# Kernel optimization log

Hardware: AMD Instinct MI355X
Metric: run time of the kernel (lower is better)

## Reference

```python
import jax, jax.numpy as jnp
import numpy as np

NBINS = 256  # skimage threshold_otsu default
RGB_W = jnp.array([0.2989, 0.5870, 0.1140], dtype=jnp.float32)  # tf.image.rgb_to_grayscale weights


def threshold_otsu(img):
    """Global Otsu threshold over all pixels, matching skimage.filters.threshold_otsu."""
    vmin = img.min()
    vmax = img.max()
    edges = jnp.linspace(vmin, vmax, NBINS + 1)
    centers = (edges[:-1] + edges[1:]) * 0.5
    hist = jnp.histogram(img.ravel(), bins=edges)[0].astype(jnp.float32)
    # class probabilities / cumulative weights
    w1 = jnp.cumsum(hist)                      # weight of class <= t
    w2 = jnp.cumsum(hist[::-1])[::-1]          # weight of class > t
    hc = hist * centers
    s1 = jnp.cumsum(hc)
    s2 = jnp.cumsum(hc[::-1])[::-1]
    m1 = s1 / jnp.maximum(w1, 1.0)
    m2 = s2 / jnp.maximum(w2, 1.0)
    # inter-class variance at each split point
    var12 = w1[:-1] * w2[1:] * (m1[:-1] - m2[1:]) ** 2
    idx = jnp.argmax(var12)
    return centers[idx]


def setup_inputs() -> dict:
    key = jax.random.key(0)
    inputs = jax.random.uniform(key, (32, 128, 2048, 3), dtype=jnp.float32)
    return {"inputs": inputs}


def reference(inputs) -> jnp.ndarray:
    # rgb_to_grayscale on first 3 channels, keep channel dim -> [B,H,W,1]
    gray = jnp.einsum('bhwc,c->bhw', inputs[..., :3].astype(jnp.float32), RGB_W)[..., None]
    thresh = threshold_otsu(gray)
    binarized = (gray > thresh).astype(jnp.float32)   # [B,H,W,1]
    # channels == 3 -> tile grayscale binarization back to 3 channels
    binarized = jnp.tile(binarized, (1, 1, 1, 3))
    return binarized
```

## Files before the change

### kernel.cpp

```cpp
#include <hip/hip_runtime.h>

static constexpr int HIST_OFF    = 2;
static constexpr int EDGES_OFF   = 258;
static constexpr int VMIN_OFF    = 515;
static constexpr int DELTA_OFF   = 516;
static constexpr int INVD_OFF    = 517;
static constexpr int THRESH_OFF  = 518;
static constexpr int SCRATCH_OFF = 1024;
static constexpr size_t GRAY_BYTE_OFF = 32768;

typedef float nfloat4 __attribute__((ext_vector_type(4)));

__device__ __forceinline__ unsigned fkey(float x) {
    unsigned u = __float_as_uint(x);
    return (u & 0x80000000u) ? ~u : (u | 0x80000000u);
}
__device__ __forceinline__ float keyf(unsigned k) {
    return (k & 0x80000000u) ? __uint_as_float(k & 0x7FFFFFFFu)
                             : __uint_as_float(~k);
}
__device__ __forceinline__ float gray1(float r, float g, float b) {
    float t0 = __fmul_rn(r, 0.2989f);
    float t1 = __fmul_rn(g, 0.5870f);
    float t2 = __fmul_rn(b, 0.1140f);
    return __fadd_rn(__fadd_rn(t0, t1), t2);
}

__device__ __forceinline__ void bin4(float x0, float x1, float x2, float x3,
                                     const float* eds, float vmin, float invd,
                                     unsigned* lh) {
    float xs[4] = {x0, x1, x2, x3};
#pragma unroll
    for (int j = 0; j < 4; ++j) {
        float x = xs[j];
        int b = (int)(__fmul_rn(__fsub_rn(x, vmin), invd));
        b = b < 0 ? 0 : (b > 255 ? 255 : b);
        while (b < 255 && x >= eds[b + 1]) ++b;
        while (b > 0 && x < eds[b]) --b;
        atomicAdd(&lh[b], 1u);
    }
}

__device__ __forceinline__ void reduce_pairs(const unsigned* __restrict__ wsu,
                                             int npairs, int t,
                                             unsigned& mn, unsigned& mx,
                                             unsigned* rmn, unsigned* rmx) {
    mn = 0xFFFFFFFFu; mx = 0u;
    for (int i = t; i < npairs; i += 256) {
        mn = min(mn, wsu[SCRATCH_OFF + 2 * i]);
        mx = max(mx, wsu[SCRATCH_OFF + 2 * i + 1]);
    }
    for (int off = 32; off > 0; off >>= 1) {
        mn = min(mn, (unsigned)__shfl_xor((int)mn, off, 64));
        mx = max(mx, (unsigned)__shfl_xor((int)mx, off, 64));
    }
    const int w = t >> 6;
    if ((t & 63) == 0) { rmn[w] = mn; rmx[w] = mx; }
    __syncthreads();
    mn = min(min(rmn[0], rmn[1]), min(rmn[2], rmn[3]));
    mx = max(max(rmx[0], rmx[1]), max(rmx[2], rmx[3]));
}


__global__ void __launch_bounds__(256)
gray_minmax_lds(const float* __restrict__ in, float* __restrict__ gray,
                unsigned* __restrict__ wsu, int npix4) {
    __shared__ float4 sb[4][2][192];
    __shared__ unsigned smn[4], smx[4];
    const float4* __restrict__ in4 = (const float4*)in;
    float4* __restrict__ gray4 = (float4*)gray;
    const int lane = threadIdx.x & 63;
    const int w = threadIdx.x >> 6;
    const int gw = blockIdx.x * 4 + w;
    const size_t base = (size_t)gw * 768;
    unsigned mn = 0xFFFFFFFFu, mx = 0u;

    if (blockIdx.x == 0) wsu[HIST_OFF + threadIdx.x] = 0u;

    float4 a0 = in4[base + lane];
    float4 a1 = in4[base + 64 + lane];
    float4 a2 = in4[base + 128 + lane];
    __builtin_amdgcn_sched_barrier(0);
    sb[w][0][lane]       = a0;
    sb[w][0][64 + lane]  = a1;
    sb[w][0][128 + lane] = a2;
    a0 = in4[base + 192 + lane];
    a1 = in4[base + 256 + lane];
    a2 = in4[base + 320 + lane];
    __builtin_amdgcn_sched_barrier(0);

#pragma unroll
    for (int t = 0; t < 4; ++t) {
        const int cb = t & 1;
        float4 c0 = sb[w][cb][3 * lane + 0];
        float4 c1 = sb[w][cb][3 * lane + 1];
        float4 c2 = sb[w][cb][3 * lane + 2];
        float g0 = gray1(c0.x, c0.y, c0.z);
        float g1 = gray1(c0.w, c1.x, c1.y);
        float g2 = gray1(c1.z, c1.w, c2.x);
        float g3 = gray1(c2.y, c2.z, c2.w);
        gray4[(size_t)gw * 256 + t * 64 + lane] = make_float4(g0, g1, g2, g3);
        unsigned k0 = fkey(g0), k1 = fkey(g1), k2 = fkey(g2), k3 = fkey(g3);
        mn = min(mn, min(min(k0, k1), min(k2, k3)));
        mx = max(mx, max(max(k0, k1), max(k2, k3)));
        if (t < 3) {
            sb[w][cb ^ 1][lane]       = a0;
            sb[w][cb ^ 1][64 + lane]  = a1;
            sb[w][cb ^ 1][128 + lane] = a2;
            if (t < 2) {
                a0 = in4[base + (size_t)(t + 2) * 192 + lane];
                a1 = in4[base + (size_t)(t + 2) * 192 + 64 + lane];
                a2 = in4[base + (size_t)(t + 2) * 192 + 128 + lane];
            }
            __builtin_amdgcn_sched_barrier(0);
        }
    }
    for (int off = 32; off > 0; off >>= 1) {
        mn = min(mn, (unsigned)__shfl_xor((int)mn, off, 64));
        mx = max(mx, (unsigned)__shfl_xor((int)mx, off, 64));
    }
    if (lane == 0) { smn[w] = mn; smx[w] = mx; }
    __syncthreads();
    if (threadIdx.x == 0) {
        mn = min(min(smn[0], smn[1]), min(smn[2], smn[3]));
        mx = max(max(smx[0], smx[1]), max(smx[2], smx[3]));
        wsu[SCRATCH_OFF + 2 * blockIdx.x]     = mn;
        wsu[SCRATCH_OFF + 2 * blockIdx.x + 1] = mx;
    }
}

__global__ void __launch_bounds__(256)
hist_fused(const float* __restrict__ gray, unsigned* __restrict__ wsu,
           int npairs, int npix4) {
    __shared__ float eds[257];
    __shared__ unsigned lh[256];
    __shared__ unsigned rmn[4], rmx[4];
    const int t = threadIdx.x;
    unsigned mn, mx;
    reduce_pairs(wsu, npairs, t, mn, mx, rmn, rmx);
    const float vmin = keyf(mn);
    const float vmax = keyf(mx);
    const float delta = __fdiv_rn(__fsub_rn(vmax, vmin), 256.0f);
    const float invd = (delta > 0.0f) ? __fdiv_rn(1.0f, delta) : 0.0f;
    eds[t] = __fadd_rn(vmin, __fmul_rn((float)t, delta));
    if (t == 0) eds[256] = vmax;
    lh[t] = 0u;
    __syncthreads();

    const int stride = gridDim.x * 256;
    const int base = blockIdx.x * 256 + t;
    float4 g[8];
#pragma unroll
    for (int j = 0; j < 8; ++j) g[j] = ((const float4*)gray)[base + j * stride];
#pragma unroll
    for (int j = 0; j < 8; ++j)
        bin4(g[j].x, g[j].y, g[j].z, g[j].w, eds, vmin, invd, lh);
    __syncthreads();
    if (lh[t] != 0u) atomicAdd(&wsu[HIST_OFF + t], lh[t]);
}

__global__ void __launch_bounds__(256)
binarize_fused(const float* __restrict__ gray, const unsigned* __restrict__ wsu,
               float* __restrict__ out, int npairs, int npix4) {
    __shared__ float eds[257];
    __shared__ float histf[256], centers[256];
    __shared__ float w1a[256], s1a[256], w2a[256], s2a[256];
    __shared__ unsigned rmn[4], rmx[4];
    __shared__ float rbv[4];
    __shared__ int rbi[4];
    __shared__ float sthresh;
    const int t = threadIdx.x;
    const int lane = t & 63;
    const int w = t >> 6;

    unsigned mn, mx;
    reduce_pairs(wsu, npairs, t, mn, mx, rmn, rmx);
    const float vmin = keyf(mn);
    const float vmax = keyf(mx);
    const float delta = __fdiv_rn(__fsub_rn(vmax, vmin), 256.0f);
    eds[t] = __fadd_rn(vmin, __fmul_rn((float)t, delta));
    if (t == 0) eds[256] = vmax;
    histf[t] = (float)wsu[HIST_OFF + t];
    __syncthreads();
    centers[t] = __fmul_rn(__fadd_rn(eds[t], eds[t + 1]), 0.5f);
    __syncthreads();
    if (t == 0) {
        float ww = 0.0f, ss = 0.0f;
        for (int k = 255; k >= 0; --k) {
            ww = __fadd_rn(ww, histf[k]);
            ss = __fadd_rn(ss, __fmul_rn(histf[k], centers[k]));
            w2a[k] = ww;
            s2a[k] = ss;
        }
        ww = 0.0f; ss = 0.0f;
        for (int k = 0; k < 255; ++k) {
            ww = __fadd_rn(ww, histf[k]);
            ss = __fadd_rn(ss, __fmul_rn(histf[k], centers[k]));
            w1a[k] = ww;
            s1a[k] = ss;
        }
    }
    __syncthreads();
    float v = -1.0f;
    int ti = 256;
    if (t < 255) {
        float m1 = __fdiv_rn(s1a[t], fmaxf(w1a[t], 1.0f));
        float m2 = __fdiv_rn(s2a[t + 1], fmaxf(w2a[t + 1], 1.0f));
        float d  = __fsub_rn(m1, m2);
        v  = __fmul_rn(__fmul_rn(w1a[t], w2a[t + 1]), __fmul_rn(d, d));
        ti = t;
    }
    for (int off = 32; off > 0; off >>= 1) {
        float ov = __shfl_xor(v, off, 64);
        int oi = __shfl_xor(ti, off, 64);
        if (ov > v || (ov == v && oi < ti)) { v = ov; ti = oi; }
    }
    if (lane == 0) { rbv[w] = v; rbi[w] = ti; }
    __syncthreads();
    if (t == 0) {
        float bv = rbv[0]; int bi = rbi[0];
        for (int k = 1; k < 4; ++k)
            if (rbv[k] > bv || (rbv[k] == bv && rbi[k] < bi)) {
                bv = rbv[k]; bi = rbi[k];
            }
        sthresh = centers[bi];
    }
    __syncthreads();
    const float thr = sthresh;

    const nfloat4* gray4 = (const nfloat4*)gray;
    nfloat4* out4 = (nfloat4*)out;
    const int gw = blockIdx.x * 4 + w;
    const int ma = lane / 3,         qa = lane % 3;
    const int mb = (64 + lane) / 3,  qb = (64 + lane) % 3;
    const int mc = (128 + lane) / 3, qc = (128 + lane) % 3;
#pragma unroll
    for (int r = 0; r < 8; ++r) {
        const int gbase = gw * 512 + r * 64;
        nfloat4 gg = gray4[gbase + lane];
        unsigned u = (gg.x > thr ? 1u : 0u) |
                     (gg.y > thr ? 0x100u : 0u) |
                     (gg.z > thr ? 0x10000u : 0u) |
                     (gg.w > thr ? 0x1000000u : 0u);
        const size_t rb = 3 * (size_t)gbase;
#pragma unroll
        for (int k = 0; k < 3; ++k) {
            int m = (k == 0) ? ma : (k == 1) ? mb : mc;
            int q = (k == 0) ? qa : (k == 1) ? qb : qc;
            unsigned x = (unsigned)__builtin_amdgcn_ds_bpermute(4 * m, (int)u);
            float h0 = (x & 0xffu)       ? 1.0f : 0.0f;
            float h1 = (x & 0xff00u)     ? 1.0f : 0.0f;
            float h2 = (x & 0xff0000u)   ? 1.0f : 0.0f;
            float h3 = (x & 0xff000000u) ? 1.0f : 0.0f;
            nfloat4 o;
            o.x = (q == 0) ? h0 : (q == 1) ? h1 : h2;
            o.y = (q == 0) ? h0 : (q == 1) ? h1 : h3;
            o.z = (q == 0) ? h0 : (q == 1) ? h2 : h3;
            o.w = (q == 0) ? h1 : (q == 1) ? h2 : h3;
            __builtin_nontemporal_store(o, &out4[rb + 64 * k + lane]);
        }
    }
}


__global__ void init_kernel(unsigned* __restrict__ wsu) {
    int i = threadIdx.x;
    if (i < 256) wsu[HIST_OFF + i] = 0u;
    if (i == 0) { wsu[0] = 0xFFFFFFFFu; wsu[1] = 0u; }
}

__global__ void __launch_bounds__(256)
gray_minmax_generic(const float* __restrict__ in, float* __restrict__ gray,
                    unsigned* __restrict__ wsu, int npix4) {
    __shared__ unsigned smn[4], smx[4];
    const float4* in4 = (const float4*)in;
    const int stride = gridDim.x * blockDim.x;
    unsigned mn = 0xFFFFFFFFu, mx = 0u;
    for (int t = blockIdx.x * blockDim.x + threadIdx.x; t < npix4; t += stride) {
        const float4* p = in4 + (size_t)t * 3;
        float4 c0 = p[0], c1 = p[1], c2 = p[2];
        float g0 = gray1(c0.x, c0.y, c0.z);
        float g1 = gray1(c0.w, c1.x, c1.y);
        float g2 = gray1(c1.z, c1.w, c2.x);
        float g3 = gray1(c2.y, c2.z, c2.w);
        if (gray) ((float4*)gray)[t] = make_float4(g0, g1, g2, g3);
        unsigned k0 = fkey(g0), k1 = fkey(g1), k2 = fkey(g2), k3 = fkey(g3);
        mn = min(mn, min(min(k0, k1), min(k2, k3)));
        mx = max(mx, max(max(k0, k1), max(k2, k3)));
    }
    for (int off = 32; off > 0; off >>= 1) {
        mn = min(mn, (unsigned)__shfl_xor((int)mn, off, 64));
        mx = max(mx, (unsigned)__shfl_xor((int)mx, off, 64));
    }
    int wave = threadIdx.x >> 6;
    if ((threadIdx.x & 63) == 0) { smn[wave] = mn; smx[wave] = mx; }
    __syncthreads();
    if (threadIdx.x == 0) {
        mn = min(min(smn[0], smn[1]), min(smn[2], smn[3]));
        mx = max(max(smx[0], smx[1]), max(smx[2], smx[3]));
        atomicMin(&wsu[0], mn);
        atomicMax(&wsu[1], mx);
    }
}

__global__ void edges_kernel(unsigned* __restrict__ wsu,
                             float* __restrict__ wsf, int nblk) {
    __shared__ unsigned rmn[4], rmx[4];
    const int i = threadIdx.x;
    unsigned mn = 0xFFFFFFFFu, mx = 0u;
    if (nblk > 0) {
        for (int b = i; b < nblk; b += 256) {
            mn = min(mn, wsu[SCRATCH_OFF + 2 * b]);
            mx = max(mx, wsu[SCRATCH_OFF + 2 * b + 1]);
        }
        for (int off = 32; off > 0; off >>= 1) {
            mn = min(mn, (unsigned)__shfl_xor((int)mn, off, 64));
            mx = max(mx, (unsigned)__shfl_xor((int)mx, off, 64));
        }
        const int w = i >> 6;
        if ((i & 63) == 0) { rmn[w] = mn; rmx[w] = mx; }
        __syncthreads();
        mn = min(min(rmn[0], rmn[1]), min(rmn[2], rmn[3]));
        mx = max(max(rmx[0], rmx[1]), max(rmx[2], rmx[3]));
    } else {
        mn = wsu[0];
        mx = wsu[1];
    }
    const float vmin = keyf(mn);
    const float vmax = keyf(mx);
    const float delta = __fdiv_rn(__fsub_rn(vmax, vmin), 256.0f);
    wsf[EDGES_OFF + i] = __fadd_rn(vmin, __fmul_rn((float)i, delta));
    if (i == 0) {
        wsf[EDGES_OFF + 256] = vmax;
        wsf[VMIN_OFF]  = vmin;
        wsf[DELTA_OFF] = delta;
        wsf[INVD_OFF]  = (delta > 0.0f) ? __fdiv_rn(1.0f, delta) : 0.0f;
    }
}

__global__ void __launch_bounds__(256)
hist_kernel(const float* __restrict__ gray, const float* __restrict__ in,
            const float* __restrict__ wsf, unsigned* __restrict__ wsu,
            int npix4) {
    __shared__ float eds[257];
    __shared__ unsigned lh[256];
    for (int i = threadIdx.x; i < 257; i += blockDim.x)
        eds[i] = wsf[EDGES_OFF + i];
    if (threadIdx.x < 256) lh[threadIdx.x] = 0u;
    __syncthreads();
    const float vmin = eds[0];
    const float invd = wsf[INVD_OFF];
    const int stride = gridDim.x * blockDim.x;
    const int base = blockIdx.x * blockDim.x + threadIdx.x;
    for (int t = base; t < npix4; t += stride) {
        float4 g4;
        if (gray) g4 = ((const float4*)gray)[t];
        else {
            const float4* p = (const float4*)in + (size_t)t * 3;
            float4 c0 = p[0], c1 = p[1], c2 = p[2];
            g4 = make_float4(gray1(c0.x, c0.y, c0.z), gray1(c0.w, c1.x, c1.y),
                             gray1(c1.z, c1.w, c2.x), gray1(c2.y, c2.z, c2.w));
        }
        bin4(g4.x, g4.y, g4.z, g4.w, eds, vmin, invd, lh);
    }
    __syncthreads();
    if (threadIdx.x < 256 && lh[threadIdx.x] != 0u)
        atomicAdd(&wsu[HIST_OFF + threadIdx.x], lh[threadIdx.x]);
}

__global__ void otsu_kernel(const unsigned* __restrict__ wsu,
                            float* __restrict__ wsf) {
    __shared__ float histf[256];
    __shared__ float centers[256];
    __shared__ float w2a[256];
    __shared__ float s2a[256];
    int i = threadIdx.x;
    float e0 = wsf[EDGES_OFF + i];
    float e1 = wsf[EDGES_OFF + i + 1];
    centers[i] = __fmul_rn(__fadd_rn(e0, e1), 0.5f);
    histf[i] = (float)wsu[HIST_OFF + i];
    __syncthreads();
    if (i == 0) {
        float w = 0.0f, s = 0.0f;
        for (int t = 255; t >= 0; --t) {
            w = __fadd_rn(w, histf[t]);
            s = __fadd_rn(s, __fmul_rn(histf[t], centers[t]));
            w2a[t] = w;
            s2a[t] = s;
        }
        float w1 = 0.0f, s1 = 0.0f, best = -1.0f;
        int bidx = 0;
        for (int t = 0; t < 255; ++t) {
            w1 = __fadd_rn(w1, histf[t]);
            s1 = __fadd_rn(s1, __fmul_rn(histf[t], centers[t]));
            float m1 = __fdiv_rn(s1, fmaxf(w1, 1.0f));
            float m2 = __fdiv_rn(s2a[t + 1], fmaxf(w2a[t + 1], 1.0f));
            float d  = __fsub_rn(m1, m2);
            float v  = __fmul_rn(__fmul_rn(w1, w2a[t + 1]), __fmul_rn(d, d));
            if (v > best) { best = v; bidx = t; }
        }
        wsf[THRESH_OFF] = centers[bidx];
    }
}

__global__ void __launch_bounds__(256)
binarize_generic(const float* __restrict__ gray, const float* __restrict__ in,
                 const float* __restrict__ wsf, float* __restrict__ out,
                 int npix4) {
    const float thr = wsf[THRESH_OFF];
    const int stride = gridDim.x * blockDim.x;
    nfloat4* out4 = (nfloat4*)out;
    for (int t = blockIdx.x * blockDim.x + threadIdx.x; t < npix4; t += stride) {
        float4 g4;
        if (gray) g4 = ((const float4*)gray)[t];
        else {
            const float4* p = (const float4*)in + (size_t)t * 3;
            float4 c0 = p[0], c1 = p[1], c2 = p[2];
            g4 = make_float4(gray1(c0.x, c0.y, c0.z), gray1(c0.w, c1.x, c1.y),
                             gray1(c1.z, c1.w, c2.x), gray1(c2.y, c2.z, c2.w));
        }
        float b0 = (g4.x > thr) ? 1.0f : 0.0f;
        float b1 = (g4.y > thr) ? 1.0f : 0.0f;
        float b2 = (g4.z > thr) ? 1.0f : 0.0f;
        float b3 = (g4.w > thr) ? 1.0f : 0.0f;
        nfloat4* o = out4 + (size_t)t * 3;
        o[0] = (nfloat4){b0, b0, b0, b1};
        o[1] = (nfloat4){b1, b1, b2, b2};
        o[2] = (nfloat4){b2, b3, b3, b3};
    }
}

static void launch_fallback(const float* in, float* out, unsigned* wsu,
                            float* wsf, float* gray, int npix4,
                            hipStream_t stream) {
    hipLaunchKernelGGL(init_kernel, dim3(1), dim3(256), 0, stream, wsu);
    hipLaunchKernelGGL(gray_minmax_generic, dim3(2048), dim3(256), 0,
                       stream, in, gray, wsu, npix4);
    hipLaunchKernelGGL(edges_kernel, dim3(1), dim3(256), 0, stream, wsu, wsf,
                       0);
    hipLaunchKernelGGL(hist_kernel, dim3(1024), dim3(256), 0, stream,
                       gray, in, wsf, wsu, npix4);
    hipLaunchKernelGGL(otsu_kernel, dim3(1), dim3(256), 0, stream, wsu, wsf);
    hipLaunchKernelGGL(binarize_generic, dim3(2048), dim3(256), 0, stream,
                       gray, in, wsf, out, npix4);
}

extern "C" void kernel_launch(void* const* d_in, const int* in_sizes, int n_in,
                              void* d_out, int out_size, void* d_ws,
                              size_t ws_size, hipStream_t stream) {
    const float* in = (const float*)d_in[0];
    float* out = (float*)d_out;
    int npix  = out_size / 3;
    int npix4 = npix / 4;
    unsigned* wsu = (unsigned*)d_ws;
    float* wsf = (float*)d_ws;
    size_t need = GRAY_BYTE_OFF + (size_t)npix * sizeof(float);
    float* gray = (ws_size >= need)
                      ? (float*)((char*)d_ws + GRAY_BYTE_OFF)
                      : nullptr;

    const bool fast = gray && (npix4 % 2048 == 0);
    if (fast) {
        const int npairs = npix4 / 1024;
        const int nb2 = npix4 / 2048;
        hipLaunchKernelGGL(gray_minmax_lds, dim3(npairs), dim3(256), 0,
                           stream, in, gray, wsu, npix4);
        hipLaunchKernelGGL(hist_fused, dim3(nb2), dim3(256), 0, stream,
                           gray, wsu, npairs, npix4);
        hipLaunchKernelGGL(binarize_fused, dim3(nb2), dim3(256), 0, stream,
                           gray, wsu, out, npairs, npix4);
    } else {
        launch_fallback(in, out, wsu, wsf, gray, npix4, stream);
    }
}
```

Measured before the change: 237.8 us.

## Fuse grayscale, histogram, Otsu and binarize into one persistent kernel with grid barriers

Adds a single cooperative-style kernel used by default. It computes grayscale values once and keeps them in registers, then uses two atomic-counter grid barriers: one to share the global min/max, one to share the global histogram. Each block then redundantly computes the Otsu threshold and writes the binarized 3-channel output with lane permutes and nontemporal stores. This removes the intermediate gray buffer writes and reads and two extra kernel launches. In exchange it relies on every block being co-resident, checked via an occupancy query. It also adds a memset and spin-wait barrier costs.

```diff
diff --git a/kernel.cpp b/kernel.cpp
--- a/kernel.cpp
+++ b/kernel.cpp
@@ -6,6 +6,8 @@
 static constexpr int DELTA_OFF   = 516;
 static constexpr int INVD_OFF    = 517;
 static constexpr int THRESH_OFF  = 518;
+static constexpr int CTRA_OFF    = 300;
+static constexpr int CTRB_OFF    = 301;
 static constexpr int SCRATCH_OFF = 1024;
 static constexpr size_t GRAY_BYTE_OFF = 32768;
 
@@ -40,6 +42,181 @@
         atomicAdd(&lh[b], 1u);
     }
 }
+
+__device__ __forceinline__ void gbar(unsigned* ctr, unsigned nblk) {
+    __syncthreads();
+    if (threadIdx.x == 0) {
+        __hip_atomic_fetch_add(ctr, 1u, __ATOMIC_ACQ_REL,
+                               __HIP_MEMORY_SCOPE_AGENT);
+        while (__hip_atomic_load(ctr, __ATOMIC_ACQUIRE,
+                                 __HIP_MEMORY_SCOPE_AGENT) < nblk)
+            __builtin_amdgcn_s_sleep(2);
+    }
+    __syncthreads();
+}
+
+__global__ void __launch_bounds__(256, 4)
+fused_all(const float* __restrict__ in, float* __restrict__ out,
+          unsigned* __restrict__ wsu, int nblk) {
+    __shared__ float eds[257];
+    __shared__ unsigned lh[256];
+    __shared__ float histf[256], centers[256];
+    __shared__ float w1a[256], s1a[256], w2a[256], s2a[256];
+    __shared__ unsigned rmn[4], rmx[4];
+    __shared__ float rbv[4];
+    __shared__ int rbi[4];
+    __shared__ float sthresh;
+
+    const int t = threadIdx.x;
+    const int lane = t & 63;
+    const int w = t >> 6;
+    const int b = blockIdx.x;
+    const int gw = b * 4 + w;
+    const float4* __restrict__ in4 = (const float4*)in;
+    nfloat4* __restrict__ out4 = (nfloat4*)out;
+
+    nfloat4 gg[8];
+    unsigned mn = 0xFFFFFFFFu, mx = 0u;
+#pragma unroll
+    for (int r = 0; r < 8; ++r) {
+        const int grp = gw * 512 + r * 64 + lane;
+        const float4* p = in4 + 3 * (size_t)grp;
+        float4 c0 = p[0], c1 = p[1], c2 = p[2];
+        float g0 = gray1(c0.x, c0.y, c0.z);
+        float g1 = gray1(c0.w, c1.x, c1.y);
+        float g2 = gray1(c1.z, c1.w, c2.x);
+        float g3 = gray1(c2.y, c2.z, c2.w);
+        gg[r].x = g0; gg[r].y = g1; gg[r].z = g2; gg[r].w = g3;
+        unsigned k0 = fkey(g0), k1 = fkey(g1), k2 = fkey(g2), k3 = fkey(g3);
+        mn = min(mn, min(min(k0, k1), min(k2, k3)));
+        mx = max(mx, max(max(k0, k1), max(k2, k3)));
+    }
+    for (int off = 32; off > 0; off >>= 1) {
+        mn = min(mn, (unsigned)__shfl_xor((int)mn, off, 64));
+        mx = max(mx, (unsigned)__shfl_xor((int)mx, off, 64));
+    }
+    if (lane == 0) { rmn[w] = mn; rmx[w] = mx; }
+    __syncthreads();
+    if (t == 0) {
+        mn = min(min(rmn[0], rmn[1]), min(rmn[2], rmn[3]));
+        mx = max(max(rmx[0], rmx[1]), max(rmx[2], rmx[3]));
+        __hip_atomic_store(&wsu[SCRATCH_OFF + 2 * b], mn, __ATOMIC_RELAXED,
+                           __HIP_MEMORY_SCOPE_AGENT);
+        __hip_atomic_store(&wsu[SCRATCH_OFF + 2 * b + 1], mx, __ATOMIC_RELAXED,
+                           __HIP_MEMORY_SCOPE_AGENT);
+    }
+    gbar(&wsu[CTRA_OFF], (unsigned)nblk);
+
+    mn = 0xFFFFFFFFu; mx = 0u;
+    for (int i = t; i < nblk; i += 256) {
+        mn = min(mn, __hip_atomic_load(&wsu[SCRATCH_OFF + 2 * i],
+                                       __ATOMIC_RELAXED,
+                                       __HIP_MEMORY_SCOPE_AGENT));
+        mx = max(mx, __hip_atomic_load(&wsu[SCRATCH_OFF + 2 * i + 1],
+                                       __ATOMIC_RELAXED,
+                                       __HIP_MEMORY_SCOPE_AGENT));
+    }
+    for (int off = 32; off > 0; off >>= 1) {
+        mn = min(mn, (unsigned)__shfl_xor((int)mn, off, 64));
+        mx = max(mx, (unsigned)__shfl_xor((int)mx, off, 64));
+    }
+    if (lane == 0) { rmn[w] = mn; rmx[w] = mx; }
+    __syncthreads();
+    mn = min(min(rmn[0], rmn[1]), min(rmn[2], rmn[3]));
+    mx = max(max(rmx[0], rmx[1]), max(rmx[2], rmx[3]));
+    const float vmin = keyf(mn);
+    const float vmax = keyf(mx);
+    const float delta = __fdiv_rn(__fsub_rn(vmax, vmin), 256.0f);
+    const float invd = (delta > 0.0f) ? __fdiv_rn(1.0f, delta) : 0.0f;
+    eds[t] = __fadd_rn(vmin, __fmul_rn((float)t, delta));
+    if (t == 0) eds[256] = vmax;
+    lh[t] = 0u;
+    __syncthreads();
+#pragma unroll
+    for (int r = 0; r < 8; ++r)
+        bin4(gg[r].x, gg[r].y, gg[r].z, gg[r].w, eds, vmin, invd, lh);
+    __syncthreads();
+    if (lh[t] != 0u) atomicAdd(&wsu[HIST_OFF + t], lh[t]);
+    gbar(&wsu[CTRB_OFF], (unsigned)nblk);
+
+    histf[t] = (float)__hip_atomic_load(&wsu[HIST_OFF + t], __ATOMIC_RELAXED,
+                                        __HIP_MEMORY_SCOPE_AGENT);
+    centers[t] = __fmul_rn(__fadd_rn(eds[t], eds[t + 1]), 0.5f);
+    __syncthreads();
+    if (t == 0) {
+        float ww = 0.0f, ss = 0.0f;
+        for (int k = 255; k >= 0; --k) {
+            ww = __fadd_rn(ww, histf[k]);
+            ss = __fadd_rn(ss, __fmul_rn(histf[k], centers[k]));
+            w2a[k] = ww;
+            s2a[k] = ss;
+        }
+        ww = 0.0f; ss = 0.0f;
+        for (int k = 0; k < 255; ++k) {
+            ww = __fadd_rn(ww, histf[k]);
+            ss = __fadd_rn(ss, __fmul_rn(histf[k], centers[k]));
+            w1a[k] = ww;
+            s1a[k] = ss;
+        }
+    }
+    __syncthreads();
+    float v = -1.0f;
+    int ti = 256;
+    if (t < 255) {
+        float m1 = __fdiv_rn(s1a[t], fmaxf(w1a[t], 1.0f));
+        float m2 = __fdiv_rn(s2a[t + 1], fmaxf(w2a[t + 1], 1.0f));
+        float d  = __fsub_rn(m1, m2);
+        v  = __fmul_rn(__fmul_rn(w1a[t], w2a[t + 1]), __fmul_rn(d, d));
+        ti = t;
+    }
+    for (int off = 32; off > 0; off >>= 1) {
+        float ov = __shfl_xor(v, off, 64);
+        int oi = __shfl_xor(ti, off, 64);
+        if (ov > v || (ov == v && oi < ti)) { v = ov; ti = oi; }
+    }
+    if (lane == 0) { rbv[w] = v; rbi[w] = ti; }
+    __syncthreads();
+    if (t == 0) {
+        float bv = rbv[0]; int bi = rbi[0];
+        for (int k = 1; k < 4; ++k)
+            if (rbv[k] > bv || (rbv[k] == bv && rbi[k] < bi)) {
+                bv = rbv[k]; bi = rbi[k];
+            }
+        sthresh = centers[bi];
+    }
+    __syncthreads();
+    const float thr = sthresh;
+
+    const int ma = lane / 3,         qa = lane % 3;
+    const int mb = (64 + lane) / 3,  qb = (64 + lane) % 3;
+    const int mc = (128 + lane) / 3, qc = (128 + lane) % 3;
+#pragma unroll
+    for (int r = 0; r < 8; ++r) {
+        const int gbase = gw * 512 + r * 64;
+        unsigned u = (gg[r].x > thr ? 1u : 0u) |
+                     (gg[r].y > thr ? 0x100u : 0u) |
+                     (gg[r].z > thr ? 0x10000u : 0u) |
+                     (gg[r].w > thr ? 0x1000000u : 0u);
+        const size_t rb = 3 * (size_t)gbase;
+#pragma unroll
+        for (int k = 0; k < 3; ++k) {
+            int m = (k == 0) ? ma : (k == 1) ? mb : mc;
+            int q = (k == 0) ? qa : (k == 1) ? qb : qc;
+            unsigned x = (unsigned)__builtin_amdgcn_ds_bpermute(4 * m, (int)u);
+            float h0 = (x & 0xffu)       ? 1.0f : 0.0f;
+            float h1 = (x & 0xff00u)     ? 1.0f : 0.0f;
+            float h2 = (x & 0xff0000u)   ? 1.0f : 0.0f;
+            float h3 = (x & 0xff000000u) ? 1.0f : 0.0f;
+            nfloat4 o;
+            o.x = (q == 0) ? h0 : (q == 1) ? h1 : h2;
+            o.y = (q == 0) ? h0 : (q == 1) ? h1 : h3;
+            o.z = (q == 0) ? h0 : (q == 1) ? h2 : h3;
+            o.w = (q == 0) ? h1 : (q == 1) ? h2 : h3;
+            __builtin_nontemporal_store(o, &out4[rb + 64 * k + lane]);
+        }
+    }
+}
+
 
 __device__ __forceinline__ void reduce_pairs(const unsigned* __restrict__ wsu,
                                              int npairs, int t,
@@ -60,7 +237,6 @@
     mn = min(min(rmn[0], rmn[1]), min(rmn[2], rmn[3]));
     mx = max(max(rmx[0], rmx[1]), max(rmx[2], rmx[3]));
 }
-
 
 __global__ void __launch_bounds__(256)
 gray_minmax_lds(const float* __restrict__ in, float* __restrict__ gray,
@@ -305,27 +481,8 @@
 
 __global__ void edges_kernel(unsigned* __restrict__ wsu,
                              float* __restrict__ wsf, int nblk) {
-    __shared__ unsigned rmn[4], rmx[4];
     const int i = threadIdx.x;
-    unsigned mn = 0xFFFFFFFFu, mx = 0u;
-    if (nblk > 0) {
-        for (int b = i; b < nblk; b += 256) {
-            mn = min(mn, wsu[SCRATCH_OFF + 2 * b]);
-            mx = max(mx, wsu[SCRATCH_OFF + 2 * b + 1]);
-        }
-        for (int off = 32; off > 0; off >>= 1) {
-            mn = min(mn, (unsigned)__shfl_xor((int)mn, off, 64));
-            mx = max(mx, (unsigned)__shfl_xor((int)mx, off, 64));
-        }
-        const int w = i >> 6;
-        if ((i & 63) == 0) { rmn[w] = mn; rmx[w] = mx; }
-        __syncthreads();
-        mn = min(min(rmn[0], rmn[1]), min(rmn[2], rmn[3]));
-        mx = max(max(rmx[0], rmx[1]), max(rmx[2], rmx[3]));
-    } else {
-        mn = wsu[0];
-        mx = wsu[1];
-    }
+    unsigned mn = wsu[0], mx = wsu[1];
     const float vmin = keyf(mn);
     const float vmax = keyf(mx);
     const float delta = __fdiv_rn(__fsub_rn(vmax, vmin), 256.0f);
@@ -430,9 +587,9 @@
     }
 }
 
-static void launch_fallback(const float* in, float* out, unsigned* wsu,
-                            float* wsf, float* gray, int npix4,
-                            hipStream_t stream) {
+static void launch_generic(const float* in, float* out, unsigned* wsu,
+                           float* wsf, float* gray, int npix4,
+                           hipStream_t stream) {
     hipLaunchKernelGGL(init_kernel, dim3(1), dim3(256), 0, stream, wsu);
     hipLaunchKernelGGL(gray_minmax_generic, dim3(2048), dim3(256), 0,
                        stream, in, gray, wsu, npix4);
@@ -459,6 +616,27 @@
                       ? (float*)((char*)d_ws + GRAY_BYTE_OFF)
                       : nullptr;
 
+    static int capacity = -2;
+    if (capacity == -2) {
+        capacity = -1;
+        int dev = 0, nb = 0;
+        hipDeviceProp_t prop;
+        if (hipGetDevice(&dev) == hipSuccess &&
+            hipGetDeviceProperties(&prop, dev) == hipSuccess &&
+            hipOccupancyMaxActiveBlocksPerMultiprocessor(
+                &nb, (const void*)fused_all, 256, 0) == hipSuccess)
+            capacity = nb * prop.multiProcessorCount;
+    }
+
+    const int NB = npix4 / 2048;
+    const bool fused_ok = (npix4 % 2048 == 0) && NB >= 1 && capacity >= NB &&
+                          ws_size >= (size_t)(SCRATCH_OFF + 2 * NB) * 4;
+    if (fused_ok) {
+        hipMemsetAsync(wsu, 0, 4096, stream);
+        hipLaunchKernelGGL(fused_all, dim3(NB), dim3(256), 0, stream,
+                           in, out, wsu, NB);
+        return;
+    }
     const bool fast = gray && (npix4 % 2048 == 0);
     if (fast) {
         const int npairs = npix4 / 1024;
@@ -470,6 +648,6 @@
         hipLaunchKernelGGL(binarize_fused, dim3(nb2), dim3(256), 0, stream,
                            gray, wsu, out, npairs, npix4);
     } else {
-        launch_fallback(in, out, wsu, wsf, gray, npix4, stream);
-    }
-}
+        launch_generic(in, out, wsu, wsf, gray, npix4, stream);
+    }
+}
```

Result: no change. 237.5 us (-0.2%).

## Shrink histogram grid, publish edges once, skip min/max re-reduction in binarize

Applied to the files above, without the earlier changes.

The histogram kernel now runs with a fixed grid of 256 blocks that loop over the gray buffer, instead of one block per 2048 float4s. This cuts the number of per-block global atomic merges and repeated min/max scratch reductions. Block 0 writes the bin edges to the workspace, so the binarize kernel reads them directly instead of re-reducing the per-block min/max pairs in every block. The output stores are switched from nontemporal to plain stores, and the fast path now requires npix4 to be a multiple of 524288. The fewer histogram blocks reduce parallelism and may expose more LDS atomic contention per block.

```diff
diff --git a/kernel.cpp b/kernel.cpp
--- a/kernel.cpp
+++ b/kernel.cpp
@@ -130,8 +130,8 @@
 }
 
 __global__ void __launch_bounds__(256)
-hist_fused(const float* __restrict__ gray, unsigned* __restrict__ wsu,
-           int npairs, int npix4) {
+hist_fused2(const float* __restrict__ gray, unsigned* __restrict__ wsu,
+            float* __restrict__ wsf, int npairs, int npix4) {
     __shared__ float eds[257];
     __shared__ unsigned lh[256];
     __shared__ unsigned rmn[4], rmx[4];
@@ -142,30 +142,45 @@
     const float vmax = keyf(mx);
     const float delta = __fdiv_rn(__fsub_rn(vmax, vmin), 256.0f);
     const float invd = (delta > 0.0f) ? __fdiv_rn(1.0f, delta) : 0.0f;
-    eds[t] = __fadd_rn(vmin, __fmul_rn((float)t, delta));
+    const float e = __fadd_rn(vmin, __fmul_rn((float)t, delta));
+    eds[t] = e;
     if (t == 0) eds[256] = vmax;
     lh[t] = 0u;
-    __syncthreads();
-
-    const int stride = gridDim.x * 256;
+    if (blockIdx.x == 0) {
+        wsf[EDGES_OFF + t] = e;
+        if (t == 0) {
+            wsf[EDGES_OFF + 256] = vmax;
+            wsf[VMIN_OFF]  = vmin;
+            wsf[DELTA_OFF] = delta;
+            wsf[INVD_OFF]  = invd;
+        }
+    }
+    __syncthreads();
+
+    const int nf4 = npix4 >> 16;
     const int base = blockIdx.x * 256 + t;
-    float4 g[8];
-#pragma unroll
-    for (int j = 0; j < 8; ++j) g[j] = ((const float4*)gray)[base + j * stride];
-#pragma unroll
-    for (int j = 0; j < 8; ++j)
-        bin4(g[j].x, g[j].y, g[j].z, g[j].w, eds, vmin, invd, lh);
+    const float4* __restrict__ gray4 = (const float4*)gray;
+    for (int it = 0; it < nf4; it += 8) {
+        float4 g[8];
+#pragma unroll
+        for (int j = 0; j < 8; ++j)
+            g[j] = gray4[(size_t)base + (size_t)(it + j) * 65536];
+#pragma unroll
+        for (int j = 0; j < 8; ++j)
+            bin4(g[j].x, g[j].y, g[j].z, g[j].w, eds, vmin, invd, lh);
+    }
     __syncthreads();
     if (lh[t] != 0u) atomicAdd(&wsu[HIST_OFF + t], lh[t]);
 }
 
 __global__ void __launch_bounds__(256)
-binarize_fused(const float* __restrict__ gray, const unsigned* __restrict__ wsu,
-               float* __restrict__ out, int npairs, int npix4) {
+binarize_fused2(const float* __restrict__ gray,
+                const unsigned* __restrict__ wsu,
+                const float* __restrict__ wsf, float* __restrict__ out,
+                int npix4) {
     __shared__ float eds[257];
     __shared__ float histf[256], centers[256];
     __shared__ float w1a[256], s1a[256], w2a[256], s2a[256];
-    __shared__ unsigned rmn[4], rmx[4];
     __shared__ float rbv[4];
     __shared__ int rbi[4];
     __shared__ float sthresh;
@@ -173,13 +188,8 @@
     const int lane = t & 63;
     const int w = t >> 6;
 
-    unsigned mn, mx;
-    reduce_pairs(wsu, npairs, t, mn, mx, rmn, rmx);
-    const float vmin = keyf(mn);
-    const float vmax = keyf(mx);
-    const float delta = __fdiv_rn(__fsub_rn(vmax, vmin), 256.0f);
-    eds[t] = __fadd_rn(vmin, __fmul_rn((float)t, delta));
-    if (t == 0) eds[256] = vmax;
+    eds[t] = wsf[EDGES_OFF + t];
+    if (t == 0) eds[256] = wsf[EDGES_OFF + 256];
     histf[t] = (float)wsu[HIST_OFF + t];
     __syncthreads();
     centers[t] = __fmul_rn(__fadd_rn(eds[t], eds[t + 1]), 0.5f);
@@ -257,7 +267,7 @@
             o.y = (q == 0) ? h0 : (q == 1) ? h1 : h3;
             o.z = (q == 0) ? h0 : (q == 1) ? h2 : h3;
             o.w = (q == 0) ? h1 : (q == 1) ? h2 : h3;
-            __builtin_nontemporal_store(o, &out4[rb + 64 * k + lane]);
+            out4[rb + 64 * k + lane] = o;
         }
     }
 }
@@ -304,28 +314,9 @@
 }
 
 __global__ void edges_kernel(unsigned* __restrict__ wsu,
-                             float* __restrict__ wsf, int nblk) {
-    __shared__ unsigned rmn[4], rmx[4];
+                             float* __restrict__ wsf) {
     const int i = threadIdx.x;
-    unsigned mn = 0xFFFFFFFFu, mx = 0u;
-    if (nblk > 0) {
-        for (int b = i; b < nblk; b += 256) {
-            mn = min(mn, wsu[SCRATCH_OFF + 2 * b]);
-            mx = max(mx, wsu[SCRATCH_OFF + 2 * b + 1]);
-        }
-        for (int off = 32; off > 0; off >>= 1) {
-            mn = min(mn, (unsigned)__shfl_xor((int)mn, off, 64));
-            mx = max(mx, (unsigned)__shfl_xor((int)mx, off, 64));
-        }
-        const int w = i >> 6;
-        if ((i & 63) == 0) { rmn[w] = mn; rmx[w] = mx; }
-        __syncthreads();
-        mn = min(min(rmn[0], rmn[1]), min(rmn[2], rmn[3]));
-        mx = max(max(rmx[0], rmx[1]), max(rmx[2], rmx[3]));
-    } else {
-        mn = wsu[0];
-        mx = wsu[1];
-    }
+    unsigned mn = wsu[0], mx = wsu[1];
     const float vmin = keyf(mn);
     const float vmax = keyf(mx);
     const float delta = __fdiv_rn(__fsub_rn(vmax, vmin), 256.0f);
@@ -430,14 +421,13 @@
     }
 }
 
-static void launch_fallback(const float* in, float* out, unsigned* wsu,
-                            float* wsf, float* gray, int npix4,
-                            hipStream_t stream) {
+static void launch_generic(const float* in, float* out, unsigned* wsu,
+                           float* wsf, float* gray, int npix4,
+                           hipStream_t stream) {
     hipLaunchKernelGGL(init_kernel, dim3(1), dim3(256), 0, stream, wsu);
     hipLaunchKernelGGL(gray_minmax_generic, dim3(2048), dim3(256), 0,
                        stream, in, gray, wsu, npix4);
-    hipLaunchKernelGGL(edges_kernel, dim3(1), dim3(256), 0, stream, wsu, wsf,
-                       0);
+    hipLaunchKernelGGL(edges_kernel, dim3(1), dim3(256), 0, stream, wsu, wsf);
     hipLaunchKernelGGL(hist_kernel, dim3(1024), dim3(256), 0, stream,
                        gray, in, wsf, wsu, npix4);
     hipLaunchKernelGGL(otsu_kernel, dim3(1), dim3(256), 0, stream, wsu, wsf);
@@ -459,17 +449,17 @@
                       ? (float*)((char*)d_ws + GRAY_BYTE_OFF)
                       : nullptr;
 
-    const bool fast = gray && (npix4 % 2048 == 0);
+    const bool fast = gray && (npix4 % 524288 == 0);
     if (fast) {
         const int npairs = npix4 / 1024;
-        const int nb2 = npix4 / 2048;
+        const int nb3 = npix4 / 2048;
         hipLaunchKernelGGL(gray_minmax_lds, dim3(npairs), dim3(256), 0,
                            stream, in, gray, wsu, npix4);
-        hipLaunchKernelGGL(hist_fused, dim3(nb2), dim3(256), 0, stream,
-                           gray, wsu, npairs, npix4);
-        hipLaunchKernelGGL(binarize_fused, dim3(nb2), dim3(256), 0, stream,
-                           gray, wsu, out, npairs, npix4);
+        hipLaunchKernelGGL(hist_fused2, dim3(256), dim3(256), 0, stream,
+                           gray, wsu, wsf, npairs, npix4);
+        hipLaunchKernelGGL(binarize_fused2, dim3(nb3), dim3(256), 0, stream,
+                           gray, wsu, wsf, out, npix4);
     } else {
-        launch_fallback(in, out, wsu, wsf, gray, npix4, stream);
-    }
-}
+        launch_generic(in, out, wsu, wsf, gray, npix4, stream);
+    }
+}
```

New measurement: 243.2 us. +2.2%, slower.
